# Optimization experiments

Hardware: AMD Instinct MI355X
Metric: run time of the kernel (lower is better)

Reference implementation:

```python
import jax, jax.numpy as jnp
import numpy as np

B, S, D, H, P = 4, 4096, 1024, 8, 32
K = D // H  # head_dim = 128


def setup_inputs() -> dict:
    key = jax.random.key(0)
    ks = jax.random.split(key, 12)
    f = lambda k, shape, s: jax.random.normal(k, shape, dtype=jnp.float32) * s
    return {
        "x": f(ks[0], (B, S, D), 1.0),
        "W_proj": f(ks[1], (H, K, D), 0.03),
        "resonance_freqs": f(ks[2], (H, K), 0.01),
        "pol_W": f(ks[3], (H, P, K), 0.08),
        "pol_b": jnp.zeros((H, P), jnp.float32),
        "imp_W1": f(ks[4], (16, 1), 0.5),               # Linear(1, 16)
        "imp_b1": jnp.zeros((16,), jnp.float32),
        "imp_W2": f(ks[5], (1, 16), 0.25),              # Linear(16, 1)
        "imp_b2": jnp.zeros((1,), jnp.float32),
        "out_W": f(ks[6], (D, D), 0.03),                # Linear(dim, dim)
        "out_b": jnp.zeros((D,), jnp.float32),
        "ln_g": jnp.ones((D,), jnp.float32),
        "ln_b": jnp.zeros((D,), jnp.float32),
        "causal": 1,
    }


def reference(x, W_proj, resonance_freqs, pol_W, pol_b, imp_W1, imp_b1,
              imp_W2, imp_b2, out_W, out_b, ln_g, ln_b, causal):
    Bx, Sx, Dx = x.shape
    nH = W_proj.shape[0]
    # per-head projection + resonance frequency modulation -> (B, H, S, K)
    heads = jnp.einsum('bsd,hkd->bhsk', x, W_proj)
    heads = heads * jnp.cos(resonance_freqs * jnp.pi)[None, :, None, :]

    # --- GuaXiangDuiChong: learned cross-head impedance ---
    summary = heads.mean(axis=2)                                   # (B, H, K)
    pol = jnp.tanh(jnp.einsum('bhk,hpk->bhp', summary, pol_W) + pol_b[None])
    pol = pol / jnp.maximum(jnp.linalg.norm(pol, axis=-1, keepdims=True), 1e-12)
    dots = jnp.einsum('bhp,bgp->bhg', pol, pol)                    # (B, H, H)
    z = dots[..., None]                                            # (B, H, H, 1)
    hid = jax.nn.gelu(z * imp_W1[:, 0] + imp_b1, approximate=False)  # (B, H, H, 16)
    imp = jax.nn.softplus(jnp.einsum('bijc,oc->bijo', hid, imp_W2) + imp_b2)[..., 0]
    eye = jnp.eye(nH, dtype=x.dtype)
    impedance = imp * (1.0 - eye)                                  # (B, H, H)

    # --- cross-head transfer ---
    # h_i += sum_{j != i} heads_j / (1 + imp[i,j]) * 0.1, causally mean-masked.
    coef = (0.1 / (1.0 + impedance)) * (1.0 - eye)                 # zero diagonal (i == j skipped)
    transfer = jnp.einsum('bij,bjsk->bisk', coef, heads)           # (B, H, S, K)
    if causal and Sx > 1:
        # masked_fill(t>s)+mean over t of a key-independent tensor == scale by (s+1)/S
        scale = (jnp.arange(Sx, dtype=x.dtype) + 1.0) / Sx
        transfer = transfer * scale[None, None, :, None]
    out_heads = heads + transfer

    merged = out_heads.transpose(0, 2, 1, 3).reshape(Bx, Sx, Dx)   # cat heads on last dim
    y = merged @ out_W.T + out_b + x                               # dropout is identity in eval
    mu = y.mean(-1, keepdims=True)
    var = ((y - mu) ** 2).mean(-1, keepdims=True)
    normed = (y - mu) / jnp.sqrt(var + 1e-5) * ln_g + ln_b
    return normed, impedance
```

## Files before the change

### kernel.cpp

```cpp
#include <hip/hip_runtime.h>

typedef __bf16 bf16x8 __attribute__((ext_vector_type(8)));
typedef float f32x4 __attribute__((ext_vector_type(4)));
typedef unsigned short us8 __attribute__((ext_vector_type(8)));

#define PI_F 3.14159265358979323846f

__device__ __forceinline__ unsigned short f2bf(float f) {
    unsigned u = __float_as_uint(f);
    u += 0x7FFFu + ((u >> 16) & 1u);
    return (unsigned short)(u >> 16);
}
__device__ __forceinline__ float bf2f(unsigned short h) {
    return __uint_as_float(((unsigned)h) << 16);
}

__device__ __forceinline__ void async16(const void* g, void* l) {
    __builtin_amdgcn_global_load_lds(
        (const __attribute__((address_space(1))) unsigned int*)g,
        (__attribute__((address_space(3))) unsigned int*)l, 16, 0, 0);
}

__global__ __launch_bounds__(256) void prep_k(const float* __restrict__ W,
                                              const float* __restrict__ fr,
                                              const float* __restrict__ Wo,
                                              unsigned short* __restrict__ W1b,
                                              unsigned short* __restrict__ Wob) {
    int idx = blockIdx.x * 256 + threadIdx.x;
    if (idx < (1 << 20)) {
        int n = idx >> 10, d = idx & 1023;
        int k = n >> 3, h = n & 7;
        float c = cosf(fr[h * 128 + k] * PI_F);
        W1b[idx] = f2bf(W[((h * 128 + k) << 10) + d] * c);
    } else {
        int i2 = idx - (1 << 20);
        int n = i2 >> 10, dp = i2 & 1023;
        int k = dp >> 3, h = dp & 7;
        Wob[i2] = f2bf(Wo[(n << 10) + h * 128 + k]);
    }
}

__global__ __launch_bounds__(256) void xbar_cast(const float* __restrict__ x,
                                                 unsigned short* __restrict__ xb,
                                                 float* __restrict__ part) {
    int bid = blockIdx.x;
    int b = bid >> 8;
    int s0 = (bid & 255) * 16;
    int t = threadIdx.x;
    float a0 = 0.f, a1 = 0.f, a2 = 0.f, a3 = 0.f;
    for (int i = 0; i < 16; ++i) {
        long row = (long)b * 4096 + s0 + i;
        float4 v = ((const float4*)x)[row * 256 + t];
        a0 += v.x; a1 += v.y; a2 += v.z; a3 += v.w;
        ushort4 u;
        u.x = f2bf(v.x); u.y = f2bf(v.y); u.z = f2bf(v.z); u.w = f2bf(v.w);
        ((ushort4*)xb)[row * 256 + t] = u;
    }
    float4 p; p.x = a0; p.y = a1; p.z = a2; p.w = a3;
    ((float4*)part)[bid * 256 + t] = p;
}

__global__ __launch_bounds__(256) void xbar_r(const float* __restrict__ part,
                                              float* __restrict__ xbar) {
    __shared__ float sl[256];
    int blk = blockIdx.x;
    int b = blk >> 3, dgrp = blk & 7;
    int t = threadIdx.x;
    int col = dgrp * 128 + (t & 127);
    int ih = t >> 7;
    float s = 0.f;
    for (int i = 0; i < 128; ++i) {
        int cb = b * 256 + ih * 128 + i;
        s += part[cb * 1024 + col];
    }
    sl[t] = s;
    __syncthreads();
    if (t < 128) xbar[b * 1024 + col] = sl[t] + sl[t + 128];
}

__global__ __launch_bounds__(256) void summary_k(const float* __restrict__ xbar,
                                                 const float* __restrict__ W,
                                                 const float* __restrict__ fr,
                                                 float* __restrict__ summary) {
    int wave = (blockIdx.x * 256 + threadIdx.x) >> 6;
    int lane = threadIdx.x & 63;
    int b = wave >> 10, hk = wave & 1023;
    int h = hk >> 7, k = hk & 127;
    const float* wrow = &W[(h * 128 + k) << 10];
    const float* xrow = &xbar[b << 10];
    float s = 0.f;
    for (int d = lane; d < 1024; d += 64) s += xrow[d] * wrow[d];
    for (int off = 32; off; off >>= 1) s += __shfl_down(s, off);
    if (lane == 0) {
        float c = cosf(fr[h * 128 + k] * PI_F);
        summary[wave] = s * c * (1.0f / 4096.0f);
    }
}

__global__ __launch_bounds__(256) void imp_k(const float* __restrict__ summary,
                                             const float* __restrict__ pol_W,
                                             const float* __restrict__ pol_b,
                                             const float* __restrict__ imp_W1,
                                             const float* __restrict__ imp_b1,
                                             const float* __restrict__ imp_W2,
                                             const float* __restrict__ imp_b2,
                                             float* __restrict__ coef_out,
                                             float* __restrict__ imp_out) {
    __shared__ float pol[4][8][32];
    __shared__ float rn[32];
    int t = threadIdx.x;
    for (int o = t; o < 1024; o += 256) {
        int b = o >> 8, h = (o >> 5) & 7, p = o & 31;
        const float* srow = &summary[(b * 8 + h) * 128];
        const float* wrow = &pol_W[(h * 32 + p) * 128];
        float acc = pol_b[h * 32 + p];
        for (int k = 0; k < 128; ++k) acc += srow[k] * wrow[k];
        pol[b][h][p] = tanhf(acc);
    }
    __syncthreads();
    if (t < 32) {
        int b = t >> 3, h = t & 7;
        float ss = 0.f;
        for (int p = 0; p < 32; ++p) { float v = pol[b][h][p]; ss += v * v; }
        rn[t] = 1.0f / fmaxf(sqrtf(ss), 1e-12f);
    }
    __syncthreads();
    {
        int b = t >> 6, i = (t >> 3) & 7, j = t & 7;
        float d = 0.f;
        for (int p = 0; p < 32; ++p) d += pol[b][i][p] * pol[b][j][p];
        d *= rn[b * 8 + i] * rn[b * 8 + j];
        float s = imp_b2[0];
        for (int c = 0; c < 16; ++c) {
            float z = d * imp_W1[c] + imp_b1[c];
            float gl = 0.5f * z * (1.0f + erff(z * 0.70710678118654752f));
            s += gl * imp_W2[c];
        }
        float sp = fmaxf(s, 0.0f) + log1pf(expf(-fabsf(s)));
        float impv = (i == j) ? 0.0f : sp;
        imp_out[t] = impv;
        coef_out[t] = (i == j) ? 0.0f : 0.1f / (1.0f + impv);
    }
}

#define VMCNT(n) asm volatile("s_waitcnt vmcnt(" #n ")" ::: "memory")
#define SBAR() __builtin_amdgcn_s_barrier()

__device__ __forceinline__ void swz256(int n, long& rowBase, long& colBase) {
    int xcd = n & 7, s = n >> 3;
    rowBase = (long)(xcd * 8 + (s & 7)) * 256;
    colBase = (long)(s >> 3) * 256;
}

#define STG(sPtr, dPtr, koff, slot)                                          \
    async16((sPtr) + (koff), (dPtr) + (slot) * 16384);                       \
    async16((sPtr) + (koff) + 262144, (dPtr) + (slot) * 16384 + 8192);

#define PH(p, DO_ST, KOFF, VM)                                               \
    {                                                                        \
        if (DO_ST) {                                                         \
            STG(sA, stDstA, (KOFF), ((p) + 2) & 3)                           \
            STG(sB, stDstB, (KOFF), ((p) + 2) & 3)                           \
        }                                                                    \
        VM;                                                                  \
        SBAR();                                                              \
        const char* pA = rdA + ((p) & 3) * 16384;                            \
        const char* pB = rdB + ((p) & 3) * 16384;                            \
        bf16x8 af[4], bv[4];                                                 \
        _Pragma("unroll") for (int i_ = 0; i_ < 4; ++i_)                     \
            af[i_] = *(const bf16x8*)(pA + i_ * 1024);                       \
        _Pragma("unroll") for (int i_ = 0; i_ < 4; ++i_)                     \
            bv[i_] = *(const bf16x8*)(pB + i_ * 1024);                       \
        __builtin_amdgcn_s_setprio(1);                                       \
        _Pragma("unroll") for (int mi = 0; mi < 4; ++mi)                     \
            _Pragma("unroll") for (int ni = 0; ni < 4; ++ni)                 \
                acc[mi][ni] = __builtin_amdgcn_mfma_f32_16x16x32_bf16(       \
                    af[mi], bv[ni], acc[mi][ni], 0, 0, 0);                   \
        __builtin_amdgcn_s_setprio(0);                                       \
        _Pragma("unroll") for (int i_ = 0; i_ < 4; ++i_)                     \
            af[i_] = *(const bf16x8*)(pA + (4 + i_) * 1024);                 \
        __builtin_amdgcn_s_setprio(1);                                       \
        _Pragma("unroll") for (int mi = 0; mi < 4; ++mi)                     \
            _Pragma("unroll") for (int ni = 0; ni < 4; ++ni)                 \
                acc[4 + mi][ni] = __builtin_amdgcn_mfma_f32_16x16x32_bf16(   \
                    af[mi], bv[ni], acc[4 + mi][ni], 0, 0, 0);               \
        __builtin_amdgcn_s_setprio(0);                                       \
    }

__device__ __forceinline__ void gemm8_core(const char* gAB, const char* gBB,
                                           char* smem, const int t,
                                           f32x4 acc[8][4]) {
    const int l = t & 63, wid = t >> 6;
    const int wm = wid >> 2, wn = wid & 3;
    const long stOff =
        (long)((wid << 4) + (l >> 2)) * 2048 + (((l & 3) ^ ((l >> 3) & 3)) * 16);
    const char* sA = gAB + stOff;
    const char* sB = gBB + stOff;
    char* As = smem;
    char* Bs = smem + 65536;
    char* stDstA = As + wid * 1024;
    char* stDstB = Bs + wid * 1024;
    const int lsw = (l & 15) * 64 + ((((l >> 4) ^ ((l >> 1) & 3))) * 16);
    const char* rdA = As + wm * 8192 + lsw;
    const char* rdB = Bs + wn * 4096 + lsw;

    STG(sA, stDstA, 0, 0)
    STG(sB, stDstB, 0, 0)
    STG(sA, stDstA, 64, 1)
    STG(sB, stDstB, 64, 1)

    int kb = 128;
    for (int grp = 0; grp < 7; ++grp) {
        PH(0, true, kb, VMCNT(8))
        PH(1, true, kb + 64, VMCNT(8))
        PH(2, true, kb + 128, VMCNT(8))
        PH(3, true, kb + 192, VMCNT(8))
        kb += 256;
    }
    PH(0, true, 1920, VMCNT(8))
    PH(1, true, 1984, VMCNT(8))
    PH(2, false, 0, VMCNT(4))
    PH(3, false, 0, VMCNT(0))
}

__global__ __launch_bounds__(512, 2) void gemm1_mix(
    const unsigned short* __restrict__ A, const unsigned short* __restrict__ B,
    const float* __restrict__ coef, const int* __restrict__ causal,
    unsigned short* __restrict__ C) {
    __shared__ char smem[131072];
    __shared__ float cfs[64];
    const int t = threadIdx.x;
    long rowBase, colBase;
    swz256(blockIdx.x, rowBase, colBase);
    const int b = (int)(rowBase >> 12);
    if (t < 64) cfs[t] = coef[b * 64 + t];
    const int causalv = causal[0];

    f32x4 acc[8][4] = {};
    gemm8_core((const char*)A + rowBase * 2048, (const char*)B + colBase * 2048,
               smem, t, acc);
    __syncthreads();

    const int l = t & 63, wid = t >> 6;
    const int wm = wid >> 2, wn = wid & 3;
    const int q = l >> 4, c16 = l & 15;
    float* slab = (float*)smem;
#pragma unroll
    for (int p = 0; p < 8; ++p) {
        if (wm == (p >> 2)) {
            const int m0 = (p & 3) * 2;
#pragma unroll
            for (int m2 = 0; m2 < 2; ++m2)
#pragma unroll
                for (int ni = 0; ni < 4; ++ni)
#pragma unroll
                    for (int r = 0; r < 4; ++r)
                        slab[(m2 * 16 + q * 4 + r) * 264 + wn * 64 + ni * 16 + c16] =
                            acc[m0 + m2][ni][r];
        }
        __syncthreads();
#pragma unroll
        for (int gg = 0; gg < 2; ++gg) {
            const int g = t + gg * 512;
            const int row32 = g >> 5, kg = g & 31;
            const float* src = slab + row32 * 264 + kg * 8;
            float v[8];
#pragma unroll
            for (int j = 0; j < 8; ++j) v[j] = src[j];
            const long row = rowBase + p * 32 + row32;
            const float scale =
                causalv ? (float)((row & 4095) + 1) * (1.0f / 4096.0f) : 1.0f;
            us8 o;
#pragma unroll
            for (int i = 0; i < 8; ++i) {
                float ts = 0.f;
#pragma unroll
                for (int j = 0; j < 8; ++j) ts += cfs[i * 8 + j] * v[j];
                o[i] = f2bf(v[i] + scale * ts);
            }
            *(us8*)(C + row * 1024 + colBase + kg * 8) = o;
        }
        __syncthreads();
    }
}

__global__ __launch_bounds__(512, 2) void gemm_bt(const unsigned short* __restrict__ A,
                                                  const unsigned short* __restrict__ B,
                                                  unsigned short* __restrict__ C) {
    __shared__ char smem[131072];
    const int t = threadIdx.x;
    long rowBase, colBase;
    swz256(blockIdx.x, rowBase, colBase);

    f32x4 acc[8][4] = {};
    gemm8_core((const char*)A + rowBase * 2048, (const char*)B + colBase * 2048,
               smem, t, acc);

    const int l = t & 63, wid = t >> 6;
    const int wm = wid >> 2, wn = wid & 3;
    const int q = l >> 4, c16 = l & 15;
#pragma unroll
    for (int mi = 0; mi < 8; ++mi)
#pragma unroll
        for (int ni = 0; ni < 4; ++ni) {
            const long col = colBase + wn * 64 + ni * 16 + c16;
            const long row0 = rowBase + wm * 128 + mi * 16 + q * 4;
#pragma unroll
            for (int r = 0; r < 4; ++r)
                C[(row0 + r) * 1024 + col] = f2bf(acc[mi][ni][r]);
        }
}

__global__ __launch_bounds__(256) void ln_k(const unsigned short* __restrict__ ypre,
                                            const float* __restrict__ x,
                                            const float* __restrict__ outb,
                                            const float* __restrict__ gam,
                                            const float* __restrict__ bet,
                                            float* __restrict__ out) {
    int row = blockIdx.x;
    int t = threadIdx.x;
    long base = (long)row * 1024 + t * 4;
    ushort4 yp = *(const ushort4*)(ypre + base);
    float4 xv = *(const float4*)(x + base);
    float4 bv = *(const float4*)(outb + t * 4);
    float y0 = bf2f(yp.x) + xv.x + bv.x;
    float y1 = bf2f(yp.y) + xv.y + bv.y;
    float y2 = bf2f(yp.z) + xv.z + bv.z;
    float y3 = bf2f(yp.w) + xv.w + bv.w;
    float s = y0 + y1 + y2 + y3;
    float ss = y0 * y0 + y1 * y1 + y2 * y2 + y3 * y3;
    for (int off = 32; off; off >>= 1) {
        s += __shfl_down(s, off);
        ss += __shfl_down(ss, off);
    }
    __shared__ float red[8];
    int wv = t >> 6, ln = t & 63;
    if (ln == 0) { red[wv] = s; red[4 + wv] = ss; }
    __syncthreads();
    float S1 = red[0] + red[1] + red[2] + red[3];
    float S2 = red[4] + red[5] + red[6] + red[7];
    float mu = S1 * (1.0f / 1024.0f);
    float var = S2 * (1.0f / 1024.0f) - mu * mu;
    float rs = 1.0f / sqrtf(var + 1e-5f);
    float4 gv = *(const float4*)(gam + t * 4);
    float4 bb = *(const float4*)(bet + t * 4);
    float4 o;
    o.x = (y0 - mu) * rs * gv.x + bb.x;
    o.y = (y1 - mu) * rs * gv.y + bb.y;
    o.z = (y2 - mu) * rs * gv.z + bb.z;
    o.w = (y3 - mu) * rs * gv.w + bb.w;
    *(float4*)(out + base) = o;
}

extern "C" void kernel_launch(void* const* d_in, const int* in_sizes, int n_in,
                              void* d_out, int out_size, void* d_ws, size_t ws_size,
                              hipStream_t stream) {
    const float* x       = (const float*)d_in[0];
    const float* W_proj  = (const float*)d_in[1];
    const float* freqs   = (const float*)d_in[2];
    const float* pol_W   = (const float*)d_in[3];
    const float* pol_b   = (const float*)d_in[4];
    const float* imp_W1  = (const float*)d_in[5];
    const float* imp_b1  = (const float*)d_in[6];
    const float* imp_W2  = (const float*)d_in[7];
    const float* imp_b2  = (const float*)d_in[8];
    const float* out_W   = (const float*)d_in[9];
    const float* out_b   = (const float*)d_in[10];
    const float* ln_g    = (const float*)d_in[11];
    const float* ln_b    = (const float*)d_in[12];
    const int*   causal  = (const int*)d_in[13];
    float* out = (float*)d_out;

    char* ws = (char*)d_ws;
    unsigned short* xb      = (unsigned short*)(ws + 0);
    unsigned short* merged  = (unsigned short*)(ws + 33554432);
    unsigned short* w1b     = (unsigned short*)(ws + 67108864);
    unsigned short* wob     = (unsigned short*)(ws + 69206016);
    float* xbar             = (float*)(ws + 71303168);
    float* summary          = (float*)(ws + 71319552);
    float* coef             = (float*)(ws + 71335936);
    float* part             = (float*)merged;
    unsigned short* ypre    = xb;

    prep_k<<<8192, 256, 0, stream>>>(W_proj, freqs, out_W, w1b, wob);
    xbar_cast<<<1024, 256, 0, stream>>>(x, xb, part);
    xbar_r<<<32, 256, 0, stream>>>(part, xbar);
    summary_k<<<1024, 256, 0, stream>>>(xbar, W_proj, freqs, summary);
    imp_k<<<1, 256, 0, stream>>>(summary, pol_W, pol_b, imp_W1, imp_b1,
                                 imp_W2, imp_b2, coef, out + 16777216);
    gemm1_mix<<<256, 512, 0, stream>>>(xb, w1b, coef, causal, merged);
    gemm_bt<<<256, 512, 0, stream>>>(merged, wob, ypre);
    ln_k<<<16384, 256, 0, stream>>>(ypre, x, out_b, ln_g, ln_b, out);
}
```

Measured before the change: 282.2 us.

## Coalesce weight prep transpose, widen imp_k, and halve epilogue slab passes

The out_W permutation in prep_k now goes through a padded LDS tile, so both the global reads and writes are vectorized and coalesced, and the grid shrinks to one block per output row. imp_k runs with 1024 threads, one polarity output each, using float4 dot products instead of looping four times per thread. The gemm1_mix epilogue stages 64 rows per pass instead of 32, giving 4 passes and fewer barriers, but it needs a larger LDS slab that must still fit in the GEMM's shared buffer.

After: 288.1 us. +2.1%, slower.

```diff
diff --git a/kernel.cpp b/kernel.cpp
--- a/kernel.cpp
+++ b/kernel.cpp
@@ -26,17 +26,28 @@
                                               const float* __restrict__ Wo,
                                               unsigned short* __restrict__ W1b,
                                               unsigned short* __restrict__ Wob) {
-    int idx = blockIdx.x * 256 + threadIdx.x;
-    if (idx < (1 << 20)) {
-        int n = idx >> 10, d = idx & 1023;
+    int bid = blockIdx.x, t = threadIdx.x;
+    if (bid < 4096) {
+        int n = bid >> 2, d = (bid & 3) * 256 + t;
         int k = n >> 3, h = n & 7;
         float c = cosf(fr[h * 128 + k] * PI_F);
-        W1b[idx] = f2bf(W[((h * 128 + k) << 10) + d] * c);
+        W1b[n * 1024 + d] = f2bf(W[((h * 128 + k) << 10) + d] * c);
     } else {
-        int i2 = idx - (1 << 20);
-        int n = i2 >> 10, dp = i2 & 1023;
-        int k = dp >> 3, h = dp & 7;
-        Wob[i2] = f2bf(Wo[(n << 10) + h * 128 + k]);
+        __shared__ float lds[1056];
+        int n = bid - 4096;
+        float4 v = ((const float4*)(Wo + (n << 10)))[t];
+        int e = t * 4;
+        *(float4*)&lds[e + (e >> 7) * 4] = v;
+        __syncthreads();
+        ushort4 o;
+        unsigned short* op = (unsigned short*)&o;
+#pragma unroll
+        for (int j = 0; j < 4; ++j) {
+            int dp = t * 4 + j;
+            int h = dp & 7, k = dp >> 3;
+            op[j] = f2bf(lds[h * 132 + k]);
+        }
+        ((ushort4*)(Wob + (n << 10)))[t] = o;
     }
 }
 
@@ -97,24 +108,27 @@
     }
 }
 
-__global__ __launch_bounds__(256) void imp_k(const float* __restrict__ summary,
-                                             const float* __restrict__ pol_W,
-                                             const float* __restrict__ pol_b,
-                                             const float* __restrict__ imp_W1,
-                                             const float* __restrict__ imp_b1,
-                                             const float* __restrict__ imp_W2,
-                                             const float* __restrict__ imp_b2,
-                                             float* __restrict__ coef_out,
-                                             float* __restrict__ imp_out) {
+__global__ __launch_bounds__(1024) void imp_k(const float* __restrict__ summary,
+                                              const float* __restrict__ pol_W,
+                                              const float* __restrict__ pol_b,
+                                              const float* __restrict__ imp_W1,
+                                              const float* __restrict__ imp_b1,
+                                              const float* __restrict__ imp_W2,
+                                              const float* __restrict__ imp_b2,
+                                              float* __restrict__ coef_out,
+                                              float* __restrict__ imp_out) {
     __shared__ float pol[4][8][32];
     __shared__ float rn[32];
     int t = threadIdx.x;
-    for (int o = t; o < 1024; o += 256) {
-        int b = o >> 8, h = (o >> 5) & 7, p = o & 31;
-        const float* srow = &summary[(b * 8 + h) * 128];
-        const float* wrow = &pol_W[(h * 32 + p) * 128];
+    {
+        int b = t >> 8, h = (t >> 5) & 7, p = t & 31;
+        const float4* srow = (const float4*)&summary[(b * 8 + h) * 128];
+        const float4* wrow = (const float4*)&pol_W[(h * 32 + p) * 128];
         float acc = pol_b[h * 32 + p];
-        for (int k = 0; k < 128; ++k) acc += srow[k] * wrow[k];
+        for (int k = 0; k < 32; ++k) {
+            float4 sv = srow[k], wv = wrow[k];
+            acc += sv.x * wv.x + sv.y * wv.y + sv.z * wv.z + sv.w * wv.w;
+        }
         pol[b][h][p] = tanhf(acc);
     }
     __syncthreads();
@@ -125,7 +139,7 @@
         rn[t] = 1.0f / fmaxf(sqrtf(ss), 1e-12f);
     }
     __syncthreads();
-    {
+    if (t < 256) {
         int b = t >> 6, i = (t >> 3) & 7, j = t & 7;
         float d = 0.f;
         for (int p = 0; p < 32; ++p) d += pol[b][i][p] * pol[b][j][p];
@@ -246,11 +260,11 @@
     const int q = l >> 4, c16 = l & 15;
     float* slab = (float*)smem;
 #pragma unroll
-    for (int p = 0; p < 8; ++p) {
-        if (wm == (p >> 2)) {
-            const int m0 = (p & 3) * 2;
-#pragma unroll
-            for (int m2 = 0; m2 < 2; ++m2)
+    for (int p = 0; p < 4; ++p) {
+        if (wm == (p >> 1)) {
+            const int m0 = (p & 1) * 4;
+#pragma unroll
+            for (int m2 = 0; m2 < 4; ++m2)
 #pragma unroll
                 for (int ni = 0; ni < 4; ++ni)
 #pragma unroll
@@ -260,14 +274,14 @@
         }
         __syncthreads();
 #pragma unroll
-        for (int gg = 0; gg < 2; ++gg) {
+        for (int gg = 0; gg < 4; ++gg) {
             const int g = t + gg * 512;
-            const int row32 = g >> 5, kg = g & 31;
-            const float* src = slab + row32 * 264 + kg * 8;
+            const int row64 = g >> 5, kg = g & 31;
+            const float* src = slab + row64 * 264 + kg * 8;
             float v[8];
 #pragma unroll
             for (int j = 0; j < 8; ++j) v[j] = src[j];
-            const long row = rowBase + p * 32 + row32;
+            const long row = rowBase + p * 64 + row64;
             const float scale =
                 causalv ? (float)((row & 4095) + 1) * (1.0f / 4096.0f) : 1.0f;
             us8 o;
@@ -382,12 +396,12 @@
     float* part             = (float*)merged;
     unsigned short* ypre    = xb;
 
-    prep_k<<<8192, 256, 0, stream>>>(W_proj, freqs, out_W, w1b, wob);
+    prep_k<<<5120, 256, 0, stream>>>(W_proj, freqs, out_W, w1b, wob);
     xbar_cast<<<1024, 256, 0, stream>>>(x, xb, part);
     xbar_r<<<32, 256, 0, stream>>>(part, xbar);
     summary_k<<<1024, 256, 0, stream>>>(xbar, W_proj, freqs, summary);
-    imp_k<<<1, 256, 0, stream>>>(summary, pol_W, pol_b, imp_W1, imp_b1,
-                                 imp_W2, imp_b2, coef, out + 16777216);
+    imp_k<<<1, 1024, 0, stream>>>(summary, pol_W, pol_b, imp_W1, imp_b1,
+                                  imp_W2, imp_b2, coef, out + 16777216);
     gemm1_mix<<<256, 512, 0, stream>>>(xb, w1b, coef, causal, merged);
     gemm_bt<<<256, 512, 0, stream>>>(merged, wob, ypre);
     ln_k<<<16384, 256, 0, stream>>>(ypre, x, out_b, ln_g, ln_b, out);
```
